# Optimization experiments

Hardware: AMD Instinct MI355X
Metric: run time of the kernel (lower is better)

## Reference

```python
import jax, jax.numpy as jnp
import numpy as np
from math import factorial, sqrt

C_CH = 8
R_BINS = 4
L_MAX = 2
MUL = C_CH * R_BINS                      # 32 channels (multiplicity) per l
DIM_IR = MUL * (L_MAX + 1) ** 2          # 288 packed irrep dim per token
PATHS = [(l1, l2, l3)
         for l1 in range(L_MAX + 1)
         for l2 in range(L_MAX + 1)
         for l3 in range(L_MAX + 1)
         if abs(l1 - l2) <= l3 <= l1 + l2]          # 15 CG paths
N_TO = [sum(1 for p in PATHS if p[2] == l3) for l3 in range(L_MAX + 1)]


def _su2_cg(j1, j2, j3):
    # complex-basis Clebsch-Gordan <j1 m1 j2 m2 | j3 m3> (integer l's, Racah formula)
    f = factorial
    M = np.zeros((2 * j1 + 1, 2 * j2 + 1, 2 * j3 + 1))
    for m1 in range(-j1, j1 + 1):
        for m2 in range(-j2, j2 + 1):
            m3 = m1 + m2
            if abs(m3) > j3:
                continue
            pref = sqrt((2 * j3 + 1) * f(j3 + j1 - j2) * f(j3 - j1 + j2)
                        * f(j1 + j2 - j3) / f(j1 + j2 + j3 + 1))
            pref *= sqrt(f(j3 + m3) * f(j3 - m3) * f(j1 - m1) * f(j1 + m1)
                         * f(j2 - m2) * f(j2 + m2))
            s = 0.0
            for k in range(j1 + j2 - j3 + 1):
                d = [k, j1 + j2 - j3 - k, j1 - m1 - k, j2 + m2 - k,
                     j3 - j2 + m1 + k, j3 - j1 - m2 + k]
                if any(v < 0 for v in d):
                    continue
                s += (-1.0) ** k / np.prod([float(f(v)) for v in d])
            M[m1 + j1, m2 + j2, m3 + j3] = pref * s
    return M


def _q(l):
    # change of basis real SH -> complex SH (e3nn convention, incl. (-i)^l phase)
    q = np.zeros((2 * l + 1, 2 * l + 1), dtype=complex)
    for m in range(-l, 0):
        q[l + m, l + abs(m)] = 1 / sqrt(2)
        q[l + m, l - abs(m)] = -1j / sqrt(2)
    q[l, l] = 1
    for m in range(1, l + 1):
        q[l + m, l + m] = (-1) ** m / sqrt(2)
        q[l + m, l - m] = 1j * (-1) ** m / sqrt(2)
    return ((-1j) ** l) * q


def _real_cg(l1, l2, l3):
    # real-basis CG tensor, unit Frobenius norm (= e3nn wigner_3j up to sign)
    C = _su2_cg(l1, l2, l3).astype(complex)
    T = np.einsum('ij,kl,mn,ikm->jln', _q(l1), _q(l2), np.conj(_q(l3)), C)
    R = np.real(T)
    if np.linalg.norm(R) < 1e-6:
        R = np.imag(T)
    return (R / np.linalg.norm(R)).astype(np.float32)


CG = [jnp.asarray(_real_cg(*p)) for p in PATHS]


def _split(x):
    # [B,N,DIM_IR] -> list of per-l blocks [B,N,MUL,2l+1] (e3nn channel-major layout)
    B, N, _ = x.shape
    blocks, off = [], 0
    for l in range(L_MAX + 1):
        sz = MUL * (2 * l + 1)
        blocks.append(x[..., off:off + sz].reshape(B, N, MUL, 2 * l + 1))
        off += sz
    return blocks


def _linear(blocks, W):
    # o3.Linear: per-l channel mix, 1/sqrt(fan_in) path normalization
    s = 1.0 / np.sqrt(MUL).astype(np.float32)
    return [jnp.einsum('bnui,uw->bnwi', blocks[l], W[l]) * s
            for l in range(L_MAX + 1)]


def _tensor_product(blocks, Wtp):
    # FullyConnectedTensorProduct(y, y): block-sparse CG contraction per path
    B, N = blocks[0].shape[:2]
    outs = [jnp.zeros((B, N, MUL, 2 * l + 1), blocks[0].dtype)
            for l in range(L_MAX + 1)]
    for p, (l1, l2, l3) in enumerate(PATHS):
        coeff = np.float32(np.sqrt((2 * l3 + 1) / (MUL * MUL * N_TO[l3])))
        # tmp: [B,N,u,v,m3]
        tmp = jnp.einsum('bnui,bnvj,ijk->bnuvk', blocks[l1], blocks[l2], CG[p])
        outs[l3] = outs[l3] + coeff * jnp.einsum('bnuvk,uvw->bnwk', tmp, Wtp[p])
    return outs


def setup_inputs() -> dict:
    key = jax.random.key(0)
    k1, k2, k3, k4 = jax.random.split(key, 4)
    B, N = 2, 4096
    return {
        'x_ir': jax.random.normal(k1, (B, N, DIM_IR), jnp.float32),
        'W1': jax.random.normal(k2, (L_MAX + 1, MUL, MUL), jnp.float32),
        'Wtp': jax.random.normal(k3, (len(PATHS), MUL, MUL, MUL), jnp.float32),
        'W2': jax.random.normal(k4, (L_MAX + 1, MUL, MUL), jnp.float32),
    }


def reference(x_ir, W1, Wtp, W2):
    B, N, _ = x_ir.shape
    y = _linear(_split(x_ir), W1)      # o3.Linear (lin1); Gate branch is dead code
    y = _tensor_product(y, Wtp)        # FullyConnectedTensorProduct(y, y)
    y = _linear(y, W2)                 # o3.Linear (lin2)
    return jnp.concatenate([b.reshape(B, N, -1) for b in y], axis=-1)
```

## Files before the change

### kernel.cpp

```cpp
#include <hip/hip_runtime.h>
#include <hip/hip_bf16.h>
#include <math.h>

#define S1f 0.17677669529663687f

typedef float  f32x4 __attribute__((ext_vector_type(4)));
typedef short  s16x8 __attribute__((ext_vector_type(8)));

struct cplx { double re, im; };
__device__ __forceinline__ cplx cmul(cplx a, cplx b){ return {a.re*b.re - a.im*b.im, a.re*b.im + a.im*b.re}; }
__device__ __forceinline__ double factd(int n){ double f=1.0; for(int i=2;i<=n;++i) f*=(double)i; return f; }

__device__ double su2cg(int j1,int j2,int j3,int m1,int m2){
  int m3 = m1+m2;
  if (m3 < -j3 || m3 > j3) return 0.0;
  double pref = sqrt((2.0*j3+1.0)*factd(j3+j1-j2)*factd(j3-j1+j2)*factd(j1+j2-j3)/factd(j1+j2+j3+1));
  pref *= sqrt(factd(j3+m3)*factd(j3-m3)*factd(j1-m1)*factd(j1+m1)*factd(j2-m2)*factd(j2+m2));
  double s = 0.0;
  for (int k=0;k<=j1+j2-j3;++k){
    int d1=j1+j2-j3-k, d2=j1-m1-k, d3=j2+m2-k, d4=j3-j2+m1+k, d5=j3-j1-m2+k;
    if (d1<0||d2<0||d3<0||d4<0||d5<0) continue;
    s += ((k&1)?-1.0:1.0)/(factd(k)*factd(d1)*factd(d2)*factd(d3)*factd(d4)*factd(d5));
  }
  return pref*s;
}

__device__ __forceinline__ cplx q_entry(int l, int r, int c){
  const double rs2 = 0.70710678118654752440;
  double re=0.0, im=0.0;
  if (r < l){
    if (c == 2*l-r) re = rs2;
    if (c == r)     im = -rs2;
  } else if (r == l){
    if (c == l) re = 1.0;
  } else {
    double sg = ((r-l)&1)?-1.0:1.0;
    if (c == r)     re = sg*rs2;
    if (c == 2*l-r) im = sg*rs2;
  }
  cplx ph;
  if (l==0)      ph = {1.0, 0.0};
  else if (l==1) ph = {0.0,-1.0};
  else           ph = {-1.0,0.0};
  return cmul(ph, (cplx){re, im});
}

__device__ const int PL[15][3] = {
 {0,0,0},{0,1,1},{0,2,2},{1,0,1},{1,1,0},{1,1,1},{1,1,2},{1,2,1},{1,2,2},
 {2,0,2},{2,1,1},{2,1,2},{2,2,0},{2,2,1},{2,2,2}};

__device__ const int OFFL[3] = {0,32,128};

template<int L1,int L2,int L3,int P>
__device__ __forceinline__ void tp_path(const float* __restrict__ y_s,
    const float* __restrict__ cg_lds, const float* __restrict__ Wtp,
    int lane, int wave, f32x4 (&acc)[9][2])
{
  constexpr int n1=2*L1+1, n2=2*L2+1, K=2*L3+1;
  constexpr int o1=(L1==0)?0:((L1==1)?32:128);
  constexpr int o2=(L2==0)?0:((L2==1)?32:128);
  constexpr int S0=(L3==0)?0:((L3==1)?1:4);
  const int t = lane&15, vg = lane>>4;
  const float* yt = y_s + t*289;
  float y2r[8][n2];
  #pragma unroll
  for (int vi=0;vi<8;++vi)
    #pragma unroll
    for (int j=0;j<n2;++j) y2r[vi][j] = yt[o2 + (vg*8+vi)*n2 + j];
  const float* cgp = cg_lds + P*128;

  #pragma unroll 1
  for (int uc=0;uc<4;++uc){
    const int u0 = wave*8 + uc*2;
    float y1r[2][n1];
    #pragma unroll
    for (int uu=0;uu<2;++uu)
      #pragma unroll
      for (int i=0;i<n1;++i) y1r[uu][i] = yt[o1 + (u0+uu)*n1 + i];
    s16x8 bfr[2][2];
    #pragma unroll
    for (int uu=0;uu<2;++uu)
      #pragma unroll
      for (int wt=0;wt<2;++wt){
        const float* wp = Wtp + (((P*32+u0+uu)*32 + vg*8)*32) + wt*16 + t;
        s16x8 b;
        #pragma unroll
        for (int j=0;j<8;++j){
          union { __hip_bfloat16 h; short s; } cv;
          cv.h = __float2bfloat16(wp[j*32]);
          b[j] = cv.s;
        }
        bfr[uu][wt] = b;
      }
    #pragma unroll
    for (int k=0;k<K;++k){
      float G[2][n2];
      #pragma unroll
      for (int uu=0;uu<2;++uu)
        #pragma unroll
        for (int j=0;j<n2;++j) G[uu][j]=0.f;
      #pragma unroll
      for (int i=0;i<n1;++i)
        #pragma unroll
        for (int j=0;j<n2;++j){
          float c = cgp[i*25 + j*5 + k];
          G[0][j] += y1r[0][i]*c;
          G[1][j] += y1r[1][i]*c;
        }
      #pragma unroll
      for (int uu=0;uu<2;++uu){
        s16x8 a;
        #pragma unroll
        for (int vi=0;vi<8;++vi){
          float af = 0.f;
          #pragma unroll
          for (int j=0;j<n2;++j) af += G[uu][j]*y2r[vi][j];
          union { __hip_bfloat16 h; short s; } cv;
          cv.h = __float2bfloat16(af);
          a[vi] = cv.s;
        }
        acc[S0+k][0] = __builtin_amdgcn_mfma_f32_16x16x32_bf16(a, bfr[uu][0], acc[S0+k][0],0,0,0);
        acc[S0+k][1] = __builtin_amdgcn_mfma_f32_16x16x32_bf16(a, bfr[uu][1], acc[S0+k][1],0,0,0);
      }
    }
  }
}

template<int L3>
__device__ __forceinline__ void lin2_group(const float* __restrict__ smem,
    const float* __restrict__ W2, int t, int sl, float* __restrict__ op)
{
  constexpr int K=2*L3+1;
  constexpr int o3=(L3==0)?0:((L3==1)?32:128);
  constexpr int B=(L3==0)?0:((L3==1)?1:4);
  float z0[K], z1[K];
  #pragma unroll
  for (int k=0;k<K;++k){ z0[k]=0.f; z1[k]=0.f; }
  const float* w2p = W2 + L3*1024 + sl*2;
  #pragma unroll 4
  for (int w=0;w<32;++w){
    float2 wv = *(const float2*)(w2p + w*32);
    #pragma unroll
    for (int k=0;k<K;++k){
      float tb = smem[(B+k)*528 + t*33 + w];
      z0[k] += tb*wv.x; z1[k] += tb*wv.y;
    }
  }
  #pragma unroll
  for (int k=0;k<K;++k){
    op[o3 + (sl*2)*K + k]   = z0[k]*S1f;
    op[o3 + (sl*2+1)*K + k] = z1[k]*S1f;
  }
}

__global__ __launch_bounds__(256,2) void sheq_main(const float* __restrict__ x,
    const float* __restrict__ W1, const float* __restrict__ Wtp,
    const float* __restrict__ W2, float* __restrict__ out)
{
  __shared__ float y_s[16*289];
  __shared__ __align__(16) float smem[4752];
  __shared__ float cg_lds[1920];

  int tid = threadIdx.x;
  int t = tid&15, sl = tid>>4;
  int lane = tid&63, wave = tid>>6;
  int tok0 = blockIdx.x*16;
  const float* xb = x + tok0*288;

  {
    double* dw  = ((double*)smem) + wave*384;
    double* Cp  = dw;
    double* TreP= dw + 128;
    double* TimP= dw + 256;
    #pragma unroll 1
    for (int c=0;c<4;++c){
      int p = c*4 + wave;
      bool act = (p < 15);
      int l1=0,l2=0,l3=0;
      if (act){ l1=PL[p][0]; l2=PL[p][1]; l3=PL[p][2]; }
      int n1=2*l1+1, n2=2*l2+1, n3=2*l3+1, tot=n1*n2*n3;
      if (act){
        for (int idx=lane; idx<tot; idx+=64){
          int i=idx/(n2*n3), r=idx-i*(n2*n3), k=r/n3, m=r-k*n3;
          Cp[idx] = ((i-l1)+(k-l2)==(m-l3)) ? su2cg(l1,l2,l3,i-l1,k-l2) : 0.0;
        }
      }
      __syncthreads();
      double pr=0.0, pim=0.0;
      if (act){
        for (int idx=lane; idx<tot; idx+=64){
          int j=idx/(n2*n3), r=idx-j*(n2*n3), L=r/n3, n=r-L*n3;
          double are=0.0, aim=0.0;
          for (int i=0;i<n1;++i) for (int k=0;k<n2;++k){
            int m=(i-l1)+(k-l2)+l3;
            if (m<0 || m>=n3) continue;
            double cv = Cp[(i*n2+k)*n3+m];
            if (cv==0.0) continue;
            cplx t1=q_entry(l1,i,j), t2=q_entry(l2,k,L), t3=q_entry(l3,m,n);
            t3.im = -t3.im;
            cplx tq = cmul(cmul(t1,t2),t3);
            are += tq.re*cv; aim += tq.im*cv;
          }
          TreP[idx]=are; TimP[idx]=aim;
          pr += are*are; pim += aim*aim;
        }
      }
      for (int off=1; off<64; off<<=1){ pr += __shfl_xor(pr,off); pim += __shfl_xor(pim,off); }
      __syncthreads();
      if (act){
        int useIm = (sqrt(pr) < 1e-6) ? 1 : 0;
        double norm = sqrt(useIm ? pim : pr);
        double co = (l3==0)? sqrt(1.0/3072.0) : ((l3==1)? sqrt(3.0/6144.0) : sqrt(5.0/6144.0));
        double scale = co/norm;
        for (int idx=lane; idx<128; idx+=64){
          float v=0.f;
          if (idx<125){
            int a=idx/25, r=idx-a*25, b=r/5, cc=r-b*5;
            if (a<n1 && b<n2 && cc<n3){
              int src=(a*n2+b)*n3+cc;
              double tv = useIm ? TimP[src] : TreP[src];
              v = (float)(tv*scale);
            }
          }
          cg_lds[p*128+idx]=v;
        }
      }
      __syncthreads();
    }
  }

  #pragma unroll
  for (int l=0;l<3;++l){
    const int nl=2*l+1, offl=OFFL[l], rl=32*nl;
    __syncthreads();
    for (int e=tid; e<16*rl; e+=256){
      int tt=e/rl, qq=e-tt*rl;
      smem[tt*161+qq]=xb[tt*288+offl+qq];
    }
    __syncthreads();
    float a0[5], a1[5];
    for (int i=0;i<nl;++i){ a0[i]=0.f; a1[i]=0.f; }
    const float* w1p = W1 + l*1024 + sl*2;
    const float* xr = smem + t*161;
    #pragma unroll 4
    for (int u=0;u<32;++u){
      float2 wv = *(const float2*)(w1p+u*32);
      for (int i=0;i<nl;++i){ float xv=xr[u*nl+i]; a0[i]+=xv*wv.x; a1[i]+=xv*wv.y; }
    }
    float* yp = y_s + t*289 + offl;
    for (int i=0;i<nl;++i){ yp[(sl*2)*nl+i]=a0[i]*S1f; yp[(sl*2+1)*nl+i]=a1[i]*S1f; }
  }
  __syncthreads();

  f32x4 acc[9][2];
  #pragma unroll
  for (int s=0;s<9;++s){ acc[s][0]=(f32x4){0.f,0.f,0.f,0.f}; acc[s][1]=(f32x4){0.f,0.f,0.f,0.f}; }

  tp_path<0,0,0, 0>(y_s,cg_lds,Wtp,lane,wave,acc);
  tp_path<0,1,1, 1>(y_s,cg_lds,Wtp,lane,wave,acc);
  tp_path<0,2,2, 2>(y_s,cg_lds,Wtp,lane,wave,acc);
  tp_path<1,0,1, 3>(y_s,cg_lds,Wtp,lane,wave,acc);
  tp_path<1,1,0, 4>(y_s,cg_lds,Wtp,lane,wave,acc);
  tp_path<1,1,1, 5>(y_s,cg_lds,Wtp,lane,wave,acc);
  tp_path<1,1,2, 6>(y_s,cg_lds,Wtp,lane,wave,acc);
  tp_path<1,2,1, 7>(y_s,cg_lds,Wtp,lane,wave,acc);
  tp_path<1,2,2, 8>(y_s,cg_lds,Wtp,lane,wave,acc);
  tp_path<2,0,2, 9>(y_s,cg_lds,Wtp,lane,wave,acc);
  tp_path<2,1,1,10>(y_s,cg_lds,Wtp,lane,wave,acc);
  tp_path<2,1,2,11>(y_s,cg_lds,Wtp,lane,wave,acc);
  tp_path<2,2,0,12>(y_s,cg_lds,Wtp,lane,wave,acc);
  tp_path<2,2,1,13>(y_s,cg_lds,Wtp,lane,wave,acc);
  tp_path<2,2,2,14>(y_s,cg_lds,Wtp,lane,wave,acc);

  for (int wv=0;wv<4;++wv){
    if (wave==wv){
      #pragma unroll
      for (int s=0;s<9;++s)
        #pragma unroll
        for (int wt=0;wt<2;++wt)
          #pragma unroll
          for (int r=0;r<4;++r){
            int row = (lane>>4)*4 + r, col = wt*16 + (lane&15);
            float* pp = &smem[s*528 + row*33 + col];
            if (wv==0) *pp = acc[s][wt][r]; else *pp += acc[s][wt][r];
          }
    }
    __syncthreads();
  }

  float* op = out + (tok0+t)*288;
  lin2_group<0>(smem, W2, t, sl, op);
  lin2_group<1>(smem, W2, t, sl, op);
  lin2_group<2>(smem, W2, t, sl, op);
}

extern "C" void kernel_launch(void* const* d_in, const int* in_sizes, int n_in,
                              void* d_out, int out_size, void* d_ws, size_t ws_size,
                              hipStream_t stream) {
  const float* x   = (const float*)d_in[0];
  const float* W1  = (const float*)d_in[1];
  const float* Wtp = (const float*)d_in[2];
  const float* W2  = (const float*)d_in[3];
  float* out = (float*)d_out;

  sheq_main<<<dim3(512), dim3(256), 0, stream>>>(x, W1, Wtp, W2, out);
}
```

Baseline: 276.6 us.

## Split tensor-product paths by output l across two blocks per token tile

Doubles the grid so each 16-token tile is handled by two blocks. One block computes the l3=0,1 paths and their lin2 outputs, the other computes the l3=2 paths. This halves the accumulator registers and shrinks the reduction smem, which should give more parallelism and occupancy on a 512-block grid. In exchange, both blocks redo the CG table construction and lin1, and the work between the two halves is uneven.

Measured after the change: 311.6 us. 1.13x slower.

```diff
diff --git a/kernel.cpp b/kernel.cpp
--- a/kernel.cpp
+++ b/kernel.cpp
@@ -51,15 +51,14 @@
 
 __device__ const int OFFL[3] = {0,32,128};
 
-template<int L1,int L2,int L3,int P>
+template<int L1,int L2,int L3,int P,int S0>
 __device__ __forceinline__ void tp_path(const float* __restrict__ y_s,
     const float* __restrict__ cg_lds, const float* __restrict__ Wtp,
-    int lane, int wave, f32x4 (&acc)[9][2])
+    int lane, int wave, f32x4 (&acc)[5][2])
 {
   constexpr int n1=2*L1+1, n2=2*L2+1, K=2*L3+1;
   constexpr int o1=(L1==0)?0:((L1==1)?32:128);
   constexpr int o2=(L2==0)?0:((L2==1)?32:128);
-  constexpr int S0=(L3==0)?0:((L3==1)?1:4);
   const int t = lane&15, vg = lane>>4;
   const float* yt = y_s + t*289;
   float y2r[8][n2];
@@ -126,13 +125,12 @@
   }
 }
 
-template<int L3>
-__device__ __forceinline__ void lin2_group(const float* __restrict__ smem,
+template<int L3,int B>
+__device__ __forceinline__ void lin2_group(const float* __restrict__ S,
     const float* __restrict__ W2, int t, int sl, float* __restrict__ op)
 {
   constexpr int K=2*L3+1;
   constexpr int o3=(L3==0)?0:((L3==1)?32:128);
-  constexpr int B=(L3==0)?0:((L3==1)?1:4);
   float z0[K], z1[K];
   #pragma unroll
   for (int k=0;k<K;++k){ z0[k]=0.f; z1[k]=0.f; }
@@ -142,7 +140,7 @@
     float2 wv = *(const float2*)(w2p + w*32);
     #pragma unroll
     for (int k=0;k<K;++k){
-      float tb = smem[(B+k)*528 + t*33 + w];
+      float tb = S[(B+k)*528 + t*33 + w];
       z0[k] += tb*wv.x; z1[k] += tb*wv.y;
     }
   }
@@ -158,14 +156,15 @@
     const float* __restrict__ W2, float* __restrict__ out)
 {
   __shared__ float y_s[16*289];
-  __shared__ __align__(16) float smem[4752];
+  __shared__ __align__(16) float smem[3072];
   __shared__ float cg_lds[1920];
 
   int tid = threadIdx.x;
   int t = tid&15, sl = tid>>4;
   int lane = tid&63, wave = tid>>6;
-  int tok0 = blockIdx.x*16;
-  const float* xb = x + tok0*288;
+  int half = blockIdx.x >> 9;
+  int tok0 = (blockIdx.x & 511) * 16;
+  const float* xb = x + (size_t)tok0*288;
 
   {
     double* dw  = ((double*)smem) + wave*384;
@@ -252,30 +251,33 @@
   }
   __syncthreads();
 
-  f32x4 acc[9][2];
-  #pragma unroll
-  for (int s=0;s<9;++s){ acc[s][0]=(f32x4){0.f,0.f,0.f,0.f}; acc[s][1]=(f32x4){0.f,0.f,0.f,0.f}; }
-
-  tp_path<0,0,0, 0>(y_s,cg_lds,Wtp,lane,wave,acc);
-  tp_path<0,1,1, 1>(y_s,cg_lds,Wtp,lane,wave,acc);
-  tp_path<0,2,2, 2>(y_s,cg_lds,Wtp,lane,wave,acc);
-  tp_path<1,0,1, 3>(y_s,cg_lds,Wtp,lane,wave,acc);
-  tp_path<1,1,0, 4>(y_s,cg_lds,Wtp,lane,wave,acc);
-  tp_path<1,1,1, 5>(y_s,cg_lds,Wtp,lane,wave,acc);
-  tp_path<1,1,2, 6>(y_s,cg_lds,Wtp,lane,wave,acc);
-  tp_path<1,2,1, 7>(y_s,cg_lds,Wtp,lane,wave,acc);
-  tp_path<1,2,2, 8>(y_s,cg_lds,Wtp,lane,wave,acc);
-  tp_path<2,0,2, 9>(y_s,cg_lds,Wtp,lane,wave,acc);
-  tp_path<2,1,1,10>(y_s,cg_lds,Wtp,lane,wave,acc);
-  tp_path<2,1,2,11>(y_s,cg_lds,Wtp,lane,wave,acc);
-  tp_path<2,2,0,12>(y_s,cg_lds,Wtp,lane,wave,acc);
-  tp_path<2,2,1,13>(y_s,cg_lds,Wtp,lane,wave,acc);
-  tp_path<2,2,2,14>(y_s,cg_lds,Wtp,lane,wave,acc);
+  f32x4 acc[5][2];
+  #pragma unroll
+  for (int s=0;s<5;++s){ acc[s][0]=(f32x4){0.f,0.f,0.f,0.f}; acc[s][1]=(f32x4){0.f,0.f,0.f,0.f}; }
+
+  if (half == 0){
+    tp_path<0,0,0, 0,0>(y_s,cg_lds,Wtp,lane,wave,acc);
+    tp_path<0,1,1, 1,1>(y_s,cg_lds,Wtp,lane,wave,acc);
+    tp_path<1,0,1, 3,1>(y_s,cg_lds,Wtp,lane,wave,acc);
+    tp_path<1,1,0, 4,0>(y_s,cg_lds,Wtp,lane,wave,acc);
+    tp_path<1,1,1, 5,1>(y_s,cg_lds,Wtp,lane,wave,acc);
+    tp_path<1,2,1, 7,1>(y_s,cg_lds,Wtp,lane,wave,acc);
+    tp_path<2,1,1,10,1>(y_s,cg_lds,Wtp,lane,wave,acc);
+    tp_path<2,2,0,12,0>(y_s,cg_lds,Wtp,lane,wave,acc);
+    tp_path<2,2,1,13,1>(y_s,cg_lds,Wtp,lane,wave,acc);
+  } else {
+    tp_path<0,2,2, 2,0>(y_s,cg_lds,Wtp,lane,wave,acc);
+    tp_path<1,1,2, 6,0>(y_s,cg_lds,Wtp,lane,wave,acc);
+    tp_path<1,2,2, 8,0>(y_s,cg_lds,Wtp,lane,wave,acc);
+    tp_path<2,0,2, 9,0>(y_s,cg_lds,Wtp,lane,wave,acc);
+    tp_path<2,1,2,11,0>(y_s,cg_lds,Wtp,lane,wave,acc);
+    tp_path<2,2,2,14,0>(y_s,cg_lds,Wtp,lane,wave,acc);
+  }
 
   for (int wv=0;wv<4;++wv){
     if (wave==wv){
       #pragma unroll
-      for (int s=0;s<9;++s)
+      for (int s=0;s<5;++s)
         #pragma unroll
         for (int wt=0;wt<2;++wt)
           #pragma unroll
@@ -288,10 +290,13 @@
     __syncthreads();
   }
 
-  float* op = out + (tok0+t)*288;
-  lin2_group<0>(smem, W2, t, sl, op);
-  lin2_group<1>(smem, W2, t, sl, op);
-  lin2_group<2>(smem, W2, t, sl, op);
+  float* op = out + (size_t)(tok0+t)*288;
+  if (half == 0){
+    lin2_group<0,0>(smem, W2, t, sl, op);
+    lin2_group<1,1>(smem, W2, t, sl, op);
+  } else {
+    lin2_group<2,0>(smem, W2, t, sl, op);
+  }
 }
 
 extern "C" void kernel_launch(void* const* d_in, const int* in_sizes, int n_in,
@@ -303,5 +308,5 @@
   const float* W2  = (const float*)d_in[3];
   float* out = (float*)d_out;
 
-  sheq_main<<<dim3(512), dim3(256), 0, stream>>>(x, W1, Wtp, W2, out);
-}
+  sheq_main<<<dim3(1024), dim3(256), 0, stream>>>(x, W1, Wtp, W2, out);
+}
```
